# Kernel tuning notes

Measured on AMD Instinct MI355X. Metric: run time of the kernel, lower is better.

## Reference

```python
import jax, jax.numpy as jnp
import numpy as np

B, D, H, L = 65536, 512, 1024, 64
LOG2PI = float(np.log(2.0 * np.pi))


def setup_inputs() -> dict:
    key = jax.random.key(0)
    ks = jax.random.split(key, 16)
    s = jnp.float32(0.02)

    def w(k, shape):
        return jax.random.normal(k, shape, dtype=jnp.float32) * s

    return {
        "x": jax.random.normal(ks[0], (B, D), dtype=jnp.float32),
        "eps": jax.random.normal(ks[1], (B, L), dtype=jnp.float32),
        # encoder params (Linear stored as [in, out] for x @ W + b)
        "W_enc_h": w(ks[2], (D, H)), "b_enc_h": jnp.zeros((H,), jnp.float32),
        "W_enc_mu": w(ks[3], (H, L)), "b_enc_mu": jnp.zeros((L,), jnp.float32),
        "W_enc_lv": w(ks[4], (H, L)), "b_enc_lv": jnp.zeros((L,), jnp.float32),
        # decoder params
        "W_dec_h": w(ks[5], (L, H)), "b_dec_h": jnp.zeros((H,), jnp.float32),
        "W_dec_mu": w(ks[6], (H, D)), "b_dec_mu": jnp.zeros((D,), jnp.float32),
        "W_dec_lv": w(ks[7], (H, D)), "b_dec_lv": jnp.zeros((D,), jnp.float32),
    }


def reference(x, eps, W_enc_h, b_enc_h, W_enc_mu, b_enc_mu, W_enc_lv, b_enc_lv,
              W_dec_h, b_dec_h, W_dec_mu, b_dec_mu, W_dec_lv, b_dec_lv):
    beta = jnp.float32(1.0)
    # encoder
    h = jnp.tanh(x @ W_enc_h + b_enc_h)                      # [B, H]
    mu_z = h @ W_enc_mu + b_enc_mu                           # [B, L]
    lv_z = h @ W_enc_lv + b_enc_lv                           # [B, L]
    # reparameterised sample
    z = mu_z + jnp.exp(0.5 * lv_z) * eps                     # [B, L]
    # decoder
    hd = jnp.tanh(z @ W_dec_h + b_dec_h)                     # [B, H]
    mu_x = jax.nn.softmax(hd @ W_dec_mu + b_dec_mu, axis=-1) # [B, D]
    lv_x = hd @ W_dec_lv + b_dec_lv                          # [B, D]
    # KL(q(z|x) || N(0, I))
    kl = -0.5 * jnp.sum(1.0 + lv_z - mu_z ** 2 - jnp.exp(lv_z), axis=-1)  # [B]
    # diagonal Gaussian log-likelihood (closed form of MultivariateNormal
    # with diag_embed(exp(ln_var)) covariance)
    ln_pxz = -0.5 * jnp.sum(lv_x + (x - mu_x) ** 2 * jnp.exp(-lv_x) + LOG2PI, axis=-1)  # [B]
    return jnp.mean(ln_pxz - beta * kl)
```

## Files before the change

### kernel.cpp

```cpp
#include <hip/hip_runtime.h>

typedef unsigned char u8;
typedef unsigned short u16;
typedef unsigned int u32;
typedef long i64;
typedef __attribute__((ext_vector_type(4))) float floatx4;

#define LOG2PI_F 1.8378770664093453f

__device__ __forceinline__ u16 f2bf(float f) {
  union { float f; u32 i; } c; c.f = f;
  u32 i = c.i;
  u32 r = (i + 0x7fffu + ((i >> 16) & 1u)) >> 16;
  return (u16)r;
}
__device__ __forceinline__ float bf2f(u16 u) {
  union { u32 i; float f; } c; c.i = ((u32)u) << 16; return c.f;
}
__device__ __forceinline__ u8 f2fp8(float f) {
  int p = __builtin_amdgcn_cvt_pk_fp8_f32(f, f, 0, false);
  return (u8)(p & 0xff);
}
__device__ __forceinline__ u32 pk4fp8(float a, float b, float c, float d) {
  int lo = __builtin_amdgcn_cvt_pk_fp8_f32(a, b, 0, false);
  int v  = __builtin_amdgcn_cvt_pk_fp8_f32(c, d, lo, true);
  return (u32)v;
}
__device__ __forceinline__ void llds16(const void* g, void* l) {
  __builtin_amdgcn_global_load_lds(
      (const __attribute__((address_space(1))) u32*)g,
      (__attribute__((address_space(3))) u32*)l, 16, 0, 0);
}

#define INV_4096  2.44140625e-4f
#define INV_16384 6.103515625e-5f

__global__ void pack_xb(const float* __restrict__ in, u32* __restrict__ out, int n4) {
  int i = blockIdx.x * 256 + threadIdx.x;
  if (i >= n4) return;
  const float4 v = ((const float4*)in)[i];
  out[i] = pk4fp8(v.x * 16.f, v.y * 16.f, v.z * 16.f, v.w * 16.f);
}

__global__ void pack_wt(const float* __restrict__ W, u8* __restrict__ Wt, int K, int N) {
  int idx = blockIdx.x * 256 + threadIdx.x;
  if (idx >= K * N) return;
  int k = idx / N, n = idx - k * N;
  Wt[(size_t)n * K + k] = f2fp8(W[idx] * 256.f);
}

__global__ void pack_wt2(const float* __restrict__ W1, const float* __restrict__ W2,
                         u8* __restrict__ Wt, int K, int N1, int N2) {
  int idx = blockIdx.x * 256 + threadIdx.x;
  if (idx >= (N1 + N2) * K) return;
  int n = idx / K, k = idx - n * K;
  float v = (n < N1) ? W1[(size_t)k * N1 + n] : W2[(size_t)k * N2 + (n - N1)];
  Wt[idx] = f2fp8(v * 256.f);
}

__global__ void catf(const float* __restrict__ a, const float* __restrict__ b,
                     float* __restrict__ o, int n1, int n2) {
  int i = blockIdx.x * 256 + threadIdx.x;
  if (i < n1) o[i] = a[i];
  else if (i < n1 + n2) o[i] = b[i - n1];
}

template <int EPI>
__global__ __launch_bounds__(256) void gemm_bt(
    const u8* __restrict__ A, const u8* __restrict__ Bt,
    const float* __restrict__ bias, void* __restrict__ Cv,
    float inv, float outs, int M, int N, int K) {
  __shared__ __align__(16) u8 As[128 * 64];
  __shared__ __align__(16) u8 Bs[128 * 64];
  const int t = threadIdx.x;
  const int wave = t >> 6, lane = t & 63;
  const int quad = lane >> 4, l16 = lane & 15;
  const int bm = blockIdx.y * 128, bn = blockIdx.x * 128;
  const int wm = (wave >> 1) * 64, wn = (wave & 1) * 64;
  const int sw = (l16 >> 2) & 3;

  floatx4 acc[4][4];
#pragma unroll
  for (int i = 0; i < 4; ++i)
#pragma unroll
    for (int j = 0; j < 4; ++j) acc[i][j] = (floatx4){0.f, 0.f, 0.f, 0.f};

  for (int kt = 0; kt < K; kt += 64) {
#pragma unroll
    for (int i = 0; i < 2; ++i) {
      int c = i * 256 + t;
      int r = c >> 2, kcS = c & 3;
      int kc = kcS ^ ((r >> 2) & 3);
      llds16(A + (size_t)(bm + r) * K + kt + kc * 16, &As[c * 16]);
      llds16(Bt + (size_t)(bn + r) * K + kt + kc * 16, &Bs[c * 16]);
    }
    __builtin_amdgcn_s_waitcnt(0);
    __syncthreads();
#pragma unroll
    for (int h = 0; h < 2; ++h) {
      i64 af[4], bfr[4];
#pragma unroll
      for (int mi = 0; mi < 4; ++mi) {
        int m = wm + mi * 16 + l16;
        af[mi] = *(const i64*)&As[(4 * m + ((2 * h + (quad >> 1)) ^ sw)) * 16 + (quad & 1) * 8];
      }
#pragma unroll
      for (int ni = 0; ni < 4; ++ni) {
        int n = wn + ni * 16 + l16;
        bfr[ni] = *(const i64*)&Bs[(4 * n + ((2 * h + (quad >> 1)) ^ sw)) * 16 + (quad & 1) * 8];
      }
#pragma unroll
      for (int mi = 0; mi < 4; ++mi)
#pragma unroll
        for (int ni = 0; ni < 4; ++ni)
          acc[mi][ni] = __builtin_amdgcn_mfma_f32_16x16x32_fp8_fp8(
              af[mi], bfr[ni], acc[mi][ni], 0, 0, 0);
    }
    __syncthreads();
  }

#pragma unroll
  for (int ni = 0; ni < 4; ++ni) {
    int col = bn + wn + ni * 16 + l16;
    float bv = bias[col];
#pragma unroll
    for (int mi = 0; mi < 4; ++mi) {
#pragma unroll
      for (int r = 0; r < 4; ++r) {
        int row = bm + wm + mi * 16 + quad * 4 + r;
        float v = acc[mi][ni][r] * inv + bv;
        if (EPI == 0) {
          ((u8*)Cv)[(size_t)row * N + col] = f2fp8(tanhf(v) * outs);
        } else {
          ((u16*)Cv)[(size_t)row * N + col] = f2bf(v);
        }
      }
    }
  }
}

__global__ __launch_bounds__(256) void gemm_z(
    const u8* __restrict__ A, const u8* __restrict__ Bt,
    const float* __restrict__ bias, const float* __restrict__ eps,
    u8* __restrict__ z, float* __restrict__ accp, int M, int K) {
  __shared__ __align__(16) u8 As[128 * 64];
  __shared__ __align__(16) u8 Bs[128 * 64];
  __shared__ float sexp[128 * 64];
  const int t = threadIdx.x;
  const int wave = t >> 6, lane = t & 63;
  const int quad = lane >> 4, l16 = lane & 15;
  const int bm = blockIdx.y * 128;
  const int wm = (wave >> 1) * 64, wn = (wave & 1) * 64;
  const int sw = (l16 >> 2) & 3;

  floatx4 acc[4][4];
#pragma unroll
  for (int i = 0; i < 4; ++i)
#pragma unroll
    for (int j = 0; j < 4; ++j) acc[i][j] = (floatx4){0.f, 0.f, 0.f, 0.f};

  for (int kt = 0; kt < K; kt += 64) {
#pragma unroll
    for (int i = 0; i < 2; ++i) {
      int c = i * 256 + t;
      int r = c >> 2, kcS = c & 3;
      int kc = kcS ^ ((r >> 2) & 3);
      llds16(A + (size_t)(bm + r) * K + kt + kc * 16, &As[c * 16]);
      llds16(Bt + (size_t)r * K + kt + kc * 16, &Bs[c * 16]);
    }
    __builtin_amdgcn_s_waitcnt(0);
    __syncthreads();
#pragma unroll
    for (int h = 0; h < 2; ++h) {
      i64 af[4], bfr[4];
#pragma unroll
      for (int mi = 0; mi < 4; ++mi) {
        int m = wm + mi * 16 + l16;
        af[mi] = *(const i64*)&As[(4 * m + ((2 * h + (quad >> 1)) ^ sw)) * 16 + (quad & 1) * 8];
      }
#pragma unroll
      for (int ni = 0; ni < 4; ++ni) {
        int n = wn + ni * 16 + l16;
        bfr[ni] = *(const i64*)&Bs[(4 * n + ((2 * h + (quad >> 1)) ^ sw)) * 16 + (quad & 1) * 8];
      }
#pragma unroll
      for (int mi = 0; mi < 4; ++mi)
#pragma unroll
        for (int ni = 0; ni < 4; ++ni)
          acc[mi][ni] = __builtin_amdgcn_mfma_f32_16x16x32_fp8_fp8(
              af[mi], bfr[ni], acc[mi][ni], 0, 0, 0);
    }
    __syncthreads();
  }

  const bool is_lv = (wave & 1);
  float kl = 0.f;
#pragma unroll
  for (int ni = 0; ni < 4; ++ni) {
    int col = wn + ni * 16 + l16;
    float bv = bias[col];
#pragma unroll
    for (int mi = 0; mi < 4; ++mi) {
#pragma unroll
      for (int r = 0; r < 4; ++r) {
        int row = wm + mi * 16 + quad * 4 + r;
        float v = acc[mi][ni][r] * INV_16384 + bv;
        if (is_lv) {
          kl += 1.0f + v - __expf(v);
          sexp[row * 64 + (col - 64)] = __expf(0.5f * v);
        } else {
          kl -= v * v;
        }
      }
    }
  }
  __syncthreads();
  if (!is_lv) {
#pragma unroll
    for (int ni = 0; ni < 4; ++ni) {
      int col = wn + ni * 16 + l16;
      float bv = bias[col];
#pragma unroll
      for (int mi = 0; mi < 4; ++mi) {
#pragma unroll
        for (int r = 0; r < 4; ++r) {
          int row = wm + mi * 16 + quad * 4 + r;
          float mu = acc[mi][ni][r] * INV_16384 + bv;
          size_t grow = (size_t)(bm + row);
          float ep = eps[grow * 64 + col];
          z[grow * 64 + col] = f2fp8((mu + sexp[row * 64 + col] * ep) * 16.f);
        }
      }
    }
  }
  kl *= 0.5f;
  for (int off = 32; off > 0; off >>= 1) kl += __shfl_xor(kl, off, 64);
  __shared__ float s4[4];
  if (lane == 0) s4[wave] = kl;
  __syncthreads();
  if (t == 0) atomicAdd(accp, s4[0] + s4[1] + s4[2] + s4[3]);
}

__global__ __launch_bounds__(256) void lik_kernel(
    const u16* __restrict__ loglv, const float* __restrict__ x,
    float* __restrict__ acc) {
  typedef __attribute__((ext_vector_type(8))) short short8;
  const int wave = threadIdx.x >> 6, lane = threadIdx.x & 63;
  float wacc = 0.f;
  for (int rr = 0; rr < 8; ++rr) {
    int row = blockIdx.x * 32 + wave * 8 + rr;
    const u16* Lr = loglv + (size_t)row * 1024;
    short8 lg8 = ((const short8*)Lr)[lane];
    float lg[8];
#pragma unroll
    for (int j = 0; j < 8; ++j) lg[j] = bf2f((u16)lg8[j]);
    float mx = lg[0];
#pragma unroll
    for (int j = 1; j < 8; ++j) mx = fmaxf(mx, lg[j]);
    for (int off = 32; off > 0; off >>= 1) mx = fmaxf(mx, __shfl_xor(mx, off, 64));
    float e[8], s = 0.f;
#pragma unroll
    for (int j = 0; j < 8; ++j) { e[j] = __expf(lg[j] - mx); s += e[j]; }
    for (int off = 32; off > 0; off >>= 1) s += __shfl_xor(s, off, 64);
    float inv_s = 1.0f / s;
    short8 lv8 = ((const short8*)Lr)[64 + lane];
    const float* xr = x + (size_t)row * 512 + lane * 8;
    float4 x0 = *(const float4*)xr, x1 = *(const float4*)(xr + 4);
    float xs[8] = {x0.x, x0.y, x0.z, x0.w, x1.x, x1.y, x1.z, x1.w};
    float T = 0.f;
#pragma unroll
    for (int j = 0; j < 8; ++j) {
      float lv = bf2f((u16)lv8[j]);
      float d = xs[j] - e[j] * inv_s;
      T += lv + d * d * __expf(-lv) + LOG2PI_F;
    }
    for (int off = 32; off > 0; off >>= 1) T += __shfl_xor(T, off, 64);
    if (lane == 0) wacc += -0.5f * T;
  }
  __shared__ float s4[4];
  if (lane == 0) s4[wave] = wacc;
  __syncthreads();
  if (threadIdx.x == 0) atomicAdd(acc, s4[0] + s4[1] + s4[2] + s4[3]);
}

__global__ void fin_kernel(const float* __restrict__ acc, float* __restrict__ out) {
  out[0] = acc[0] * (1.0f / 65536.0f);
}

extern "C" void kernel_launch(void* const* d_in, const int* in_sizes, int n_in,
                              void* d_out, int out_size, void* d_ws, size_t ws_size,
                              hipStream_t stream) {
  const int B = 65536, D = 512, H = 1024, L = 64;
  const float* x       = (const float*)d_in[0];
  const float* eps     = (const float*)d_in[1];
  const float* W_enc_h = (const float*)d_in[2];
  const float* b_enc_h = (const float*)d_in[3];
  const float* W_enc_mu= (const float*)d_in[4];
  const float* b_enc_mu= (const float*)d_in[5];
  const float* W_enc_lv= (const float*)d_in[6];
  const float* b_enc_lv= (const float*)d_in[7];
  const float* W_dec_h = (const float*)d_in[8];
  const float* b_dec_h = (const float*)d_in[9];
  const float* W_dec_mu= (const float*)d_in[10];
  const float* b_dec_mu= (const float*)d_in[11];
  const float* W_dec_lv= (const float*)d_in[12];
  const float* b_dec_lv= (const float*)d_in[13];

  char* ws = (char*)d_ws;
  u8*   Wt_eh  = (u8*)(ws + 0);
  u8*   Wt_z   = (u8*)(ws + 524288);
  u8*   Wt_dh  = (u8*)(ws + 655360);
  u8*   Wt_dx  = (u8*)(ws + 720896);
  float* bh    = (float*)(ws + 2097152);
  float* bz    = (float*)(ws + 2101248);
  float* bdh   = (float*)(ws + 2105344);
  float* bdx   = (float*)(ws + 2109440);
  float* acc   = (float*)(ws + 2113536);
  u8*   hbuf   = (u8*)(ws + 4194304);
  u8*   xb     = (u8*)(ws + 71303168);
  u8*   zbuf   = (u8*)(ws + 104857600);
  u16*  loglv  = (u16*)(ws + 109051904);

  hipMemsetAsync(acc, 0, 256, stream);

  pack_xb<<<(B * D / 4 + 255) / 256, 256, 0, stream>>>(x, (u32*)xb, B * D / 4);
  pack_wt<<<(D * H + 255) / 256, 256, 0, stream>>>(W_enc_h, Wt_eh, D, H);
  pack_wt2<<<(H * 2 * L + 255) / 256, 256, 0, stream>>>(W_enc_mu, W_enc_lv, Wt_z, H, L, L);
  pack_wt<<<(L * H + 255) / 256, 256, 0, stream>>>(W_dec_h, Wt_dh, L, H);
  pack_wt2<<<(H * 2 * D + 255) / 256, 256, 0, stream>>>(W_dec_mu, W_dec_lv, Wt_dx, H, D, D);
  catf<<<(H + 255) / 256, 256, 0, stream>>>(b_enc_h, b_enc_h, bh, H, 0);
  catf<<<(2 * L + 255) / 256, 256, 0, stream>>>(b_enc_mu, b_enc_lv, bz, L, L);
  catf<<<(H + 255) / 256, 256, 0, stream>>>(b_dec_h, b_dec_h, bdh, H, 0);
  catf<<<(2 * D + 255) / 256, 256, 0, stream>>>(b_dec_mu, b_dec_lv, bdx, D, D);

  gemm_bt<0><<<dim3(H / 128, B / 128), 256, 0, stream>>>(
      xb, Wt_eh, bh, hbuf, INV_4096, 64.f, B, H, D);
  gemm_z<<<dim3(1, B / 128), 256, 0, stream>>>(hbuf, Wt_z, bz, eps, zbuf, acc, B, H);
  gemm_bt<0><<<dim3(H / 128, B / 128), 256, 0, stream>>>(
      zbuf, Wt_dh, bdh, hbuf, INV_4096, 64.f, B, H, L);
  gemm_bt<2><<<dim3(1024 / 128, B / 128), 256, 0, stream>>>(
      hbuf, Wt_dx, bdx, loglv, INV_16384, 0.f, B, 1024, H);
  lik_kernel<<<B / 32, 256, 0, stream>>>(loglv, x, acc);
  fin_kernel<<<1, 1, 0, stream>>>(acc, (float*)d_out);
}
```

Measured before the change: 628.3 us.

## Permute K within 64-chunks so each lane loads 16-byte MFMA fragments

Reorders the K dimension inside every 64-element chunk of all packed fp8 operands (inputs, weights, and the intermediate activations written by the epilogues). With this ordering each lane fetches both halves of its MFMA fragment in one 16-byte LDS read instead of two 8-byte reads, and the LDS swizzle is changed to match. The goal is fewer LDS read instructions and less bank conflict traffic in the GEMM inner loop. The cost is scattered byte stores in the epilogues and pack kernels, and correctness relies on every producer and consumer using the same permutation.

Result: no change. 619.0 us (-1.5%).

```diff
diff --git a/kernel.cpp b/kernel.cpp
--- a/kernel.cpp
+++ b/kernel.cpp
@@ -4,6 +4,7 @@
 typedef unsigned short u16;
 typedef unsigned int u32;
 typedef long i64;
+typedef __attribute__((ext_vector_type(2))) long long2v;
 typedef __attribute__((ext_vector_type(4))) float floatx4;
 
 #define LOG2PI_F 1.8378770664093453f
@@ -31,6 +32,11 @@
       (const __attribute__((address_space(1))) u32*)g,
       (__attribute__((address_space(3))) u32*)l, 16, 0, 0);
 }
+__device__ __forceinline__ u32 permk(u32 k) {
+  u32 g = k & ~63u, o = (k >> 3) & 7u, r = k & 7u;
+  u32 po = ((o & 3u) << 1) | (o >> 2);
+  return g | (po << 3) | r;
+}
 
 #define INV_4096  2.44140625e-4f
 #define INV_16384 6.103515625e-5f
@@ -39,14 +45,17 @@
   int i = blockIdx.x * 256 + threadIdx.x;
   if (i >= n4) return;
   const float4 v = ((const float4*)in)[i];
-  out[i] = pk4fp8(v.x * 16.f, v.y * 16.f, v.z * 16.f, v.w * 16.f);
+  int row = i >> 7;
+  int k = (i & 127) << 2;
+  int kp = permk(k);
+  out[(row << 7) + (kp >> 2)] = pk4fp8(v.x * 16.f, v.y * 16.f, v.z * 16.f, v.w * 16.f);
 }
 
 __global__ void pack_wt(const float* __restrict__ W, u8* __restrict__ Wt, int K, int N) {
   int idx = blockIdx.x * 256 + threadIdx.x;
   if (idx >= K * N) return;
   int k = idx / N, n = idx - k * N;
-  Wt[(size_t)n * K + k] = f2fp8(W[idx] * 256.f);
+  Wt[(size_t)n * K + permk(k)] = f2fp8(W[idx] * 256.f);
 }
 
 __global__ void pack_wt2(const float* __restrict__ W1, const float* __restrict__ W2,
@@ -55,7 +64,7 @@
   if (idx >= (N1 + N2) * K) return;
   int n = idx / K, k = idx - n * K;
   float v = (n < N1) ? W1[(size_t)k * N1 + n] : W2[(size_t)k * N2 + (n - N1)];
-  Wt[idx] = f2fp8(v * 256.f);
+  Wt[(size_t)n * K + permk(k)] = f2fp8(v * 256.f);
 }
 
 __global__ void catf(const float* __restrict__ a, const float* __restrict__ b,
@@ -77,7 +86,6 @@
   const int quad = lane >> 4, l16 = lane & 15;
   const int bm = blockIdx.y * 128, bn = blockIdx.x * 128;
   const int wm = (wave >> 1) * 64, wn = (wave & 1) * 64;
-  const int sw = (l16 >> 2) & 3;
 
   floatx4 acc[4][4];
 #pragma unroll
@@ -90,32 +98,32 @@
     for (int i = 0; i < 2; ++i) {
       int c = i * 256 + t;
       int r = c >> 2, kcS = c & 3;
-      int kc = kcS ^ ((r >> 2) & 3);
+      int kc = kcS ^ ((r >> 1) & 3);
       llds16(A + (size_t)(bm + r) * K + kt + kc * 16, &As[c * 16]);
       llds16(Bt + (size_t)(bn + r) * K + kt + kc * 16, &Bs[c * 16]);
     }
     __builtin_amdgcn_s_waitcnt(0);
     __syncthreads();
-#pragma unroll
-    for (int h = 0; h < 2; ++h) {
-      i64 af[4], bfr[4];
-#pragma unroll
-      for (int mi = 0; mi < 4; ++mi) {
-        int m = wm + mi * 16 + l16;
-        af[mi] = *(const i64*)&As[(4 * m + ((2 * h + (quad >> 1)) ^ sw)) * 16 + (quad & 1) * 8];
-      }
-#pragma unroll
-      for (int ni = 0; ni < 4; ++ni) {
-        int n = wn + ni * 16 + l16;
-        bfr[ni] = *(const i64*)&Bs[(4 * n + ((2 * h + (quad >> 1)) ^ sw)) * 16 + (quad & 1) * 8];
-      }
+
+    long2v a2[4], b2[4];
+#pragma unroll
+    for (int mi = 0; mi < 4; ++mi) {
+      int m = wm + mi * 16 + l16;
+      a2[mi] = *(const long2v*)&As[(4 * m + (quad ^ ((m >> 1) & 3))) * 16];
+    }
+#pragma unroll
+    for (int ni = 0; ni < 4; ++ni) {
+      int n = wn + ni * 16 + l16;
+      b2[ni] = *(const long2v*)&Bs[(4 * n + (quad ^ ((n >> 1) & 3))) * 16];
+    }
+#pragma unroll
+    for (int h = 0; h < 2; ++h)
 #pragma unroll
       for (int mi = 0; mi < 4; ++mi)
 #pragma unroll
         for (int ni = 0; ni < 4; ++ni)
           acc[mi][ni] = __builtin_amdgcn_mfma_f32_16x16x32_fp8_fp8(
-              af[mi], bfr[ni], acc[mi][ni], 0, 0, 0);
-    }
+              a2[mi][h], b2[ni][h], acc[mi][ni], 0, 0, 0);
     __syncthreads();
   }
 
@@ -130,7 +138,7 @@
         int row = bm + wm + mi * 16 + quad * 4 + r;
         float v = acc[mi][ni][r] * inv + bv;
         if (EPI == 0) {
-          ((u8*)Cv)[(size_t)row * N + col] = f2fp8(tanhf(v) * outs);
+          ((u8*)Cv)[(size_t)row * N + permk(col)] = f2fp8(tanhf(v) * outs);
         } else {
           ((u16*)Cv)[(size_t)row * N + col] = f2bf(v);
         }
@@ -151,7 +159,6 @@
   const int quad = lane >> 4, l16 = lane & 15;
   const int bm = blockIdx.y * 128;
   const int wm = (wave >> 1) * 64, wn = (wave & 1) * 64;
-  const int sw = (l16 >> 2) & 3;
 
   floatx4 acc[4][4];
 #pragma unroll
@@ -164,32 +171,32 @@
     for (int i = 0; i < 2; ++i) {
       int c = i * 256 + t;
       int r = c >> 2, kcS = c & 3;
-      int kc = kcS ^ ((r >> 2) & 3);
+      int kc = kcS ^ ((r >> 1) & 3);
       llds16(A + (size_t)(bm + r) * K + kt + kc * 16, &As[c * 16]);
       llds16(Bt + (size_t)r * K + kt + kc * 16, &Bs[c * 16]);
     }
     __builtin_amdgcn_s_waitcnt(0);
     __syncthreads();
-#pragma unroll
-    for (int h = 0; h < 2; ++h) {
-      i64 af[4], bfr[4];
-#pragma unroll
-      for (int mi = 0; mi < 4; ++mi) {
-        int m = wm + mi * 16 + l16;
-        af[mi] = *(const i64*)&As[(4 * m + ((2 * h + (quad >> 1)) ^ sw)) * 16 + (quad & 1) * 8];
-      }
-#pragma unroll
-      for (int ni = 0; ni < 4; ++ni) {
-        int n = wn + ni * 16 + l16;
-        bfr[ni] = *(const i64*)&Bs[(4 * n + ((2 * h + (quad >> 1)) ^ sw)) * 16 + (quad & 1) * 8];
-      }
+
+    long2v a2[4], b2[4];
+#pragma unroll
+    for (int mi = 0; mi < 4; ++mi) {
+      int m = wm + mi * 16 + l16;
+      a2[mi] = *(const long2v*)&As[(4 * m + (quad ^ ((m >> 1) & 3))) * 16];
+    }
+#pragma unroll
+    for (int ni = 0; ni < 4; ++ni) {
+      int n = wn + ni * 16 + l16;
+      b2[ni] = *(const long2v*)&Bs[(4 * n + (quad ^ ((n >> 1) & 3))) * 16];
+    }
+#pragma unroll
+    for (int h = 0; h < 2; ++h)
 #pragma unroll
       for (int mi = 0; mi < 4; ++mi)
 #pragma unroll
         for (int ni = 0; ni < 4; ++ni)
           acc[mi][ni] = __builtin_amdgcn_mfma_f32_16x16x32_fp8_fp8(
-              af[mi], bfr[ni], acc[mi][ni], 0, 0, 0);
-    }
+              a2[mi][h], b2[ni][h], acc[mi][ni], 0, 0, 0);
     __syncthreads();
   }
 
@@ -228,7 +235,7 @@
           float mu = acc[mi][ni][r] * INV_16384 + bv;
           size_t grow = (size_t)(bm + row);
           float ep = eps[grow * 64 + col];
-          z[grow * 64 + col] = f2fp8((mu + sexp[row * 64 + col] * ep) * 16.f);
+          z[grow * 64 + permk(col)] = f2fp8((mu + sexp[row * 64 + col] * ep) * 16.f);
         }
       }
     }
```
